# Performance work log

Hardware: AMD Instinct MI355X
Metric: run time of the kernel (lower is better)

The kernel has to match this reference:

```python
import jax, jax.numpy as jnp
import numpy as np

HEAD_SIZE = 64
EMBED_DIM = 1024
N_HEAD = EMBED_DIM // HEAD_SIZE
BATCH, SEQ = 8, 2048


def wkv6(r, k, v, w, u, s):
    # r,k,v,w: (B,T,H,D); u: (H,D); s: (B,H,D,D) indexed state[j,i] (j: key dim, i: value dim)
    decay = jnp.exp(-jnp.exp(w))  # RWKV-6 CUDA kernel computes exp(-exp(w)) per channel/step

    def step(state, inp):
        r_t, k_t, v_t, d_t = inp  # each (B,H,D)
        kv = k_t[..., :, None] * v_t[..., None, :]  # (B,H,D,D)
        y_t = jnp.einsum('bhj,bhji->bhi', r_t, state + u[..., :, None] * kv)
        state = d_t[..., :, None] * state + kv
        return state, y_t

    xs = tuple(jnp.moveaxis(t, 1, 0) for t in (r, k, v, decay))  # time-major (T,B,H,D)
    s_final, y = jax.lax.scan(step, s, xs)
    return jnp.moveaxis(y, 0, 1), s_final  # (B,T,H,D), (B,H,D,D)


def setup_inputs() -> dict:
    key = jax.random.key(0)
    ks = jax.random.split(key, 20)
    C, H, D = EMBED_DIM, N_HEAD, HEAD_SIZE
    f = jnp.float32
    inp = {
        'x': jax.random.normal(ks[0], (BATCH, SEQ, C), f),
        'x_last': jax.random.normal(ks[1], (BATCH, SEQ, C), f),
        's': jnp.zeros((BATCH, H, D, D), f),
        'miu_x': jax.random.uniform(ks[2], (1, 1, C), f),
        'lambda_': jax.random.uniform(ks[3], (5, 1, 1, C), f),
        'A': jax.random.normal(ks[4], (C, 160), f) * 0.01,
        'B_lora': jax.random.normal(ks[5], (5, 32, C), f) * 0.01,
        'time_decay_miu': jax.random.uniform(ks[6], (1, 1, C), f, minval=-6.0, maxval=-0.5),
        'td_A': jax.random.normal(ks[7], (C, 64), f) * 0.01,
        'td_B': jax.random.normal(ks[8], (64, C), f) * 0.01,
        'u': jax.random.normal(ks[9], (H, D), f) * 0.5,
        'W_k': jax.random.normal(ks[10], (C, C), f) * (0.05 / C ** 0.5),
        'W_v': jax.random.normal(ks[11], (C, C), f) * (0.5 / C ** 0.5),
        'W_r': jax.random.normal(ks[12], (C, C), f) * (0.5 / C ** 0.5),
        'W_o': jax.random.normal(ks[13], (C, C), f) * (0.5 / C ** 0.5),
        'W_g1': jax.random.normal(ks[14], (C, 160), f) * 0.01,
        'W_g2': jax.random.normal(ks[15], (160, C), f) * 0.01,
        'gn_gamma': jnp.ones((C,), f),
        'gn_beta': jnp.zeros((C,), f),
    }
    return inp


def reference(x, x_last, s, miu_x, lambda_, A, B_lora, time_decay_miu, td_A, td_B, u,
              W_k, W_v, W_r, W_o, W_g1, W_g2, gn_gamma, gn_beta):
    Bsz, T, C = x.shape
    H, D = C // HEAD_SIZE, HEAD_SIZE
    x_raw = x
    # ddlerp: token-shift mix with data-dependent mus from batched LoRA
    b_a = x_last - x
    xl = x + b_a * miu_x
    # NB: source uses a raw .view(5, B*T, 32) (no transpose) -- replicate exactly with reshape
    t1 = jnp.tanh(xl @ A).reshape(5, Bsz * T, 32)
    miu = lambda_ + jnp.einsum('fmk,fkc->fmc', t1, B_lora).reshape(5, Bsz, T, C)
    xdd = x[None] + b_a[None] * miu  # (5,B,T,C)
    w0, k0, v0, r0, g0 = xdd[0], xdd[1], xdd[2], xdd[3], xdd[4]
    # decay LoRA
    w = time_decay_miu + jnp.tanh(w0 @ td_A) @ td_B  # (B,T,C)
    k = (k0 @ W_k.T) * jnp.exp(jnp.minimum(w, 0.0))
    v = v0 @ W_v.T
    r = r0 @ W_r.T
    g = jnp.tanh(g0 @ W_g1) @ W_g2
    rh, kh, vh, wh = (t.reshape(Bsz, T, H, D) for t in (r, k, v, w))
    y, s_new = wkv6(rh, kh, vh, wh, u, s)
    # GroupNorm over (B*T, n_head groups of head_size), eps = 1e-5 * n_head
    y = y.reshape(Bsz * T, H, D)
    eps = 1e-5 * H
    mu = y.mean(axis=-1, keepdims=True)
    var = y.var(axis=-1, keepdims=True)
    yn = (y - mu) / jnp.sqrt(var + eps)
    yn = yn * gn_gamma.reshape(H, D) + gn_beta.reshape(H, D)
    yn = yn.reshape(Bsz, T, C)
    out = (yn * g) @ W_o.T
    return out, x_raw, s_new
```

## Files before the change

kernel.cpp:

```cpp
#include <hip/hip_runtime.h>
#include <hip/hip_bf16.h>

namespace {

typedef __attribute__((ext_vector_type(8))) short short8x;
typedef __attribute__((ext_vector_type(4))) float f32x4;

__device__ __forceinline__ float bf2f(unsigned short h) {
    return __uint_as_float(((unsigned int)h) << 16);
}
__device__ __forceinline__ unsigned short f2bf(float f) {
    __hip_bfloat16 h = __float2bfloat16(f);
    return *reinterpret_cast<unsigned short*>(&h);
}

enum { ACT_NONE = 0, ACT_TANH = 1 };
enum { EPI_NONE = 0, EPI_KSCALE = 1, EPI_ADDVEC = 2 };

template <int ACT, int EPI, int SBF>
__launch_bounds__(256) __global__
void gemm_mfma(int Npad, int K, int Nreal, int Cstride,
               const unsigned short* __restrict__ A,
               const unsigned short* __restrict__ B,
               float* __restrict__ Cf, unsigned short* __restrict__ Cb,
               const float* __restrict__ epi)
{
    __shared__ unsigned short as_[128 * 32];
    __shared__ unsigned short bs_[128 * 32];
    const int tid = threadIdx.x;
    const int lane = tid & 63;
    const int wave = tid >> 6;
    const int m0 = blockIdx.y << 7;
    const int n0 = blockIdx.x << 7;
    const int wm = (wave >> 1) << 6;
    const int wn = (wave & 1) << 6;

    f32x4 acc[4][4];
    const f32x4 zero = {0.f, 0.f, 0.f, 0.f};
#pragma unroll
    for (int i = 0; i < 4; ++i)
#pragma unroll
        for (int j = 0; j < 4; ++j) acc[i][j] = zero;

    const int sr = tid >> 2;
    const int sc4 = tid & 3;

    for (int k0 = 0; k0 < K; k0 += 32) {
        const uint4 a0 = *(const uint4*)(A + (size_t)(m0 + sr) * K + k0 + sc4 * 8);
        const uint4 a1 = *(const uint4*)(A + (size_t)(m0 + 64 + sr) * K + k0 + sc4 * 8);
        const uint4 b0 = *(const uint4*)(B + (size_t)(n0 + sr) * K + k0 + sc4 * 8);
        const uint4 b1 = *(const uint4*)(B + (size_t)(n0 + 64 + sr) * K + k0 + sc4 * 8);
        __syncthreads();
        {
            int r = sr, p = sc4 ^ ((r >> 1) & 3);
            *(uint4*)&as_[r * 32 + p * 8] = a0;
            *(uint4*)&bs_[r * 32 + p * 8] = b0;
            r = 64 + sr; p = sc4 ^ ((r >> 1) & 3);
            *(uint4*)&as_[r * 32 + p * 8] = a1;
            *(uint4*)&bs_[r * 32 + p * 8] = b1;
        }
        __syncthreads();
        const int q = lane >> 4;
        const int l15 = lane & 15;
        short8x af[4], bfr[4];
#pragma unroll
        for (int i = 0; i < 4; ++i) {
            const int m = wm + (i << 4) + l15;
            const int pa = q ^ ((m >> 1) & 3);
            af[i] = *(const short8x*)&as_[m * 32 + pa * 8];
            const int n = wn + (i << 4) + l15;
            const int pb = q ^ ((n >> 1) & 3);
            bfr[i] = *(const short8x*)&bs_[n * 32 + pb * 8];
        }
#pragma unroll
        for (int i = 0; i < 4; ++i)
#pragma unroll
            for (int j = 0; j < 4; ++j)
                acc[i][j] = __builtin_amdgcn_mfma_f32_16x16x32_bf16(af[i], bfr[j], acc[i][j], 0, 0, 0);
    }

    const int q = lane >> 4;
    const int cn = lane & 15;
#pragma unroll
    for (int i = 0; i < 4; ++i) {
#pragma unroll
        for (int j = 0; j < 4; ++j) {
#pragma unroll
            for (int rr = 0; rr < 4; ++rr) {
                const int row = m0 + wm + (i << 4) + (q << 2) + rr;
                const int col = n0 + wn + (j << 4) + cn;
                if (col >= Nreal) continue;
                float v = acc[i][j][rr];
                if constexpr (ACT == ACT_TANH) v = tanhf(v);
                if constexpr (EPI == EPI_KSCALE)
                    v *= __expf(fminf(epi[(size_t)row * 1024 + col], 0.f));
                if constexpr (EPI == EPI_ADDVEC) v += epi[col];
                if constexpr (SBF) Cb[(size_t)row * Cstride + col] = f2bf(v);
                else               Cf[(size_t)row * Cstride + col] = v;
            }
        }
    }
}

__launch_bounds__(256) __global__
void mix_k(const float* __restrict__ x, const float* __restrict__ xla,
           const float* __restrict__ mux, unsigned short* __restrict__ out)
{
    const size_t idx = ((size_t)blockIdx.x * 256 + threadIdx.x) * 4;
    const int c = (int)(idx & 1023);
    const float4 xv = *(const float4*)(x + idx);
    const float4 xl = *(const float4*)(xla + idx);
    const float4 mu = *(const float4*)(mux + c);
    ushort4 o;
    o.x = f2bf(xv.x + (xl.x - xv.x) * mu.x);
    o.y = f2bf(xv.y + (xl.y - xv.y) * mu.y);
    o.z = f2bf(xv.z + (xl.z - xv.z) * mu.z);
    o.w = f2bf(xv.w + (xl.w - xv.w) * mu.w);
    *(ushort4*)(out + idx) = o;
}

__launch_bounds__(256) __global__
void convert_k(const float* __restrict__ src, unsigned short* __restrict__ dst)
{
    const size_t idx = ((size_t)blockIdx.x * 256 + threadIdx.x) * 4;
    const float4 v = *(const float4*)(src + idx);
    ushort4 o;
    o.x = f2bf(v.x); o.y = f2bf(v.y); o.z = f2bf(v.z); o.w = f2bf(v.w);
    *(ushort4*)(dst + idx) = o;
}

__launch_bounds__(256) __global__
void transpose_k(const float* __restrict__ src, unsigned short* __restrict__ dst,
                 int K, int Nsrc)
{
    const int k = blockIdx.x * 256 + threadIdx.x;
    const int n = blockIdx.y;
    if (k < K)
        dst[(size_t)n * K + k] = (n < Nsrc) ? f2bf(src[(size_t)k * Nsrc + n]) : (unsigned short)0;
}

__launch_bounds__(256) __global__
void xdd_k(const float* __restrict__ x, const float* __restrict__ xla,
           const unsigned short* __restrict__ t1, const float* __restrict__ blora,
           const float* __restrict__ lam, unsigned short* __restrict__ out, int f)
{
    __shared__ float sh[4][32];
    const int tid = threadIdx.x;
    const int m0 = blockIdx.x << 2;
    if (tid < 128) {
        const int r = tid >> 5, kk = tid & 31;
        sh[r][kk] = bf2f(t1[(size_t)f * 524288 + (size_t)(m0 + r) * 32 + kk]);
    }
    __syncthreads();
    const int c0 = tid << 2;
    const float* bl = blora + f * 32768 + c0;
    float dot[4][4];
#pragma unroll
    for (int r = 0; r < 4; ++r)
#pragma unroll
        for (int j = 0; j < 4; ++j) dot[r][j] = 0.f;
    for (int kk = 0; kk < 32; ++kk) {
        const float4 b4 = *(const float4*)(bl + (size_t)kk * 1024);
#pragma unroll
        for (int r = 0; r < 4; ++r) {
            const float tv = sh[r][kk];
            dot[r][0] = fmaf(tv, b4.x, dot[r][0]);
            dot[r][1] = fmaf(tv, b4.y, dot[r][1]);
            dot[r][2] = fmaf(tv, b4.z, dot[r][2]);
            dot[r][3] = fmaf(tv, b4.w, dot[r][3]);
        }
    }
    const float4 l4 = *(const float4*)(lam + f * 1024 + c0);
#pragma unroll
    for (int r = 0; r < 4; ++r) {
        const size_t idx = (size_t)(m0 + r) * 1024 + c0;
        const float4 xv = *(const float4*)(x + idx);
        const float4 xl = *(const float4*)(xla + idx);
        ushort4 o;
        o.x = f2bf(xv.x + (xl.x - xv.x) * (l4.x + dot[r][0]));
        o.y = f2bf(xv.y + (xl.y - xv.y) * (l4.y + dot[r][1]));
        o.z = f2bf(xv.z + (xl.z - xv.z) * (l4.z + dot[r][2]));
        o.w = f2bf(xv.w + (xl.w - xv.w) * (l4.w + dot[r][3]));
        *(ushort4*)(out + idx) = o;
    }
}

__launch_bounds__(256) __global__
void zero_k(float4* __restrict__ p)
{
    const float4 z = {0.f, 0.f, 0.f, 0.f};
    p[(size_t)blockIdx.x * 256 + threadIdx.x] = z;
}

#define WKV_LOAD(RX, KX, WX, VV, T0)                                          \
    do {                                                                      \
        const size_t ti_ = tbase + (size_t)((T0) + ttl) * 1024;               \
        RX = r[ti_]; KX = k[ti_]; WX = w[ti_];                                \
        _Pragma("unroll")                                                     \
        for (int tt = 0; tt < 8; ++tt)                                        \
            VV[tt] = v[cbase + (size_t)((T0) + tt) * 1024];                   \
    } while (0)

#define WKV_CHUNK(RX, KX, WX, VV, T0)                                         \
    do {                                                                      \
        const float rr_ = bf2f(RX);                                           \
        const float kk_ = bf2f(KX);                                           \
        const float dd_ = __expf(-__expf(WX));                                \
        float4 tup_;                                                          \
        tup_.x = rr_; tup_.y = kk_; tup_.z = dd_; tup_.w = rr_ * kk_ * uj;    \
        __builtin_amdgcn_wave_barrier();    \
        sh[l] = tup_;                                                         \
        __builtin_amdgcn_wave_barrier();        \
        _Pragma("unroll")                                                     \
        for (int tt = 0; tt < 8; ++tt) {                                      \
            const float vi_ = bf2f(VV[tt]);                                   \
            float ya0_ = 0.f, ya1_ = 0.f, yb_ = 0.f;                          \
            _Pragma("unroll")                                                 \
            for (int jj = 0; jj < 8; ++jj) {                                  \
                const float4 t4_ = sh[(tt << 3) + jj];                        \
                const float sj_ = s[jj];                                      \
                if (jj & 1) ya1_ = fmaf(t4_.x, sj_, ya1_);                    \
                else        ya0_ = fmaf(t4_.x, sj_, ya0_);                    \
                yb_ += t4_.w;                                                 \
                s[jj] = fmaf(t4_.z, sj_, t4_.y * vi_);                        \
            }                                                                 \
            unsafeAtomicAdd(&y[cbase + (size_t)((T0) + tt) * 1024],           \
                            ya0_ + ya1_ + yb_ * vi_);                         \
        }                                                                     \
    } while (0)

__launch_bounds__(64) __global__
void wkv_k(const unsigned short* __restrict__ r, const unsigned short* __restrict__ k,
           const unsigned short* __restrict__ v, const float* __restrict__ w,
           const float* __restrict__ u, const float* __restrict__ s_in,
           float* __restrict__ y, float* __restrict__ s_out)
{
    const int blk = blockIdx.x;
    const int bh = blk >> 3;
    const int jc = blk & 7;
    const int h = bh & 15;
    const int l = threadIdx.x;
    const int jbase = jc << 3;

    float s[8];
    const size_t sb = (size_t)bh * 4096;
#pragma unroll
    for (int jj = 0; jj < 8; ++jj) s[jj] = s_in[sb + (size_t)(jbase + jj) * 64 + l];

    const int ttl = l >> 3;
    const int jl = l & 7;
    const float uj = u[(h << 6) + jbase + jl];

    __shared__ float4 sh[64];

    const size_t cbase = (size_t)(bh >> 4) * (2048 * 1024) + (h << 6) + l;
    const size_t tbase = (size_t)(bh >> 4) * (2048 * 1024) + (h << 6) + jbase + jl;

    unsigned short rA, kA; float wA; unsigned short vA[8];
    unsigned short rB, kB; float wB; unsigned short vB[8];

    WKV_LOAD(rA, kA, wA, vA, 0);
    for (int c = 0; c < 256; c += 2) {
        WKV_LOAD(rB, kB, wB, vB, (c + 1) * 8);
        WKV_CHUNK(rA, kA, wA, vA, c * 8);
        if (c + 2 < 256) WKV_LOAD(rA, kA, wA, vA, (c + 2) * 8);
        WKV_CHUNK(rB, kB, wB, vB, (c + 1) * 8);
    }
#pragma unroll
    for (int jj = 0; jj < 8; ++jj) s_out[sb + (size_t)(jbase + jj) * 64 + l] = s[jj];
}

__launch_bounds__(256) __global__
void gn_k(const float* __restrict__ y0,
          const unsigned short* __restrict__ g, const float* __restrict__ gam,
          const float* __restrict__ bet, unsigned short* __restrict__ z)
{
    const int tid = threadIdx.x;
    const size_t row = blockIdx.x;
    const int c0 = tid << 2;
    const size_t idx = row * 1024 + c0;
    const float4 a = *(const float4*)(y0 + idx);
    const float yv0 = a.x, yv1 = a.y, yv2 = a.z, yv3 = a.w;
    float sm = yv0 + yv1 + yv2 + yv3;
    float q = yv0 * yv0 + yv1 * yv1 + yv2 * yv2 + yv3 * yv3;
#pragma unroll
    for (int off = 1; off < 16; off <<= 1) {
        sm += __shfl_xor(sm, off, 64);
        q += __shfl_xor(q, off, 64);
    }
    const float mean = sm * (1.f / 64.f);
    const float var = q * (1.f / 64.f) - mean * mean;
    const float rstd = rsqrtf(var + 1.6e-4f);
    const float4 gm = *(const float4*)(gam + c0);
    const float4 bt = *(const float4*)(bet + c0);
    const ushort4 gg = *(const ushort4*)(g + idx);
    ushort4 o;
    o.x = f2bf(((yv0 - mean) * rstd * gm.x + bt.x) * bf2f(gg.x));
    o.y = f2bf(((yv1 - mean) * rstd * gm.y + bt.y) * bf2f(gg.y));
    o.z = f2bf(((yv2 - mean) * rstd * gm.z + bt.z) * bf2f(gg.z));
    o.w = f2bf(((yv3 - mean) * rstd * gm.w + bt.w) * bf2f(gg.w));
    *(ushort4*)(z + idx) = o;
}

__launch_bounds__(256) __global__
void copy_k(const float4* __restrict__ src, float4* __restrict__ dst)
{
    const size_t i = (size_t)blockIdx.x * 256 + threadIdx.x;
    dst[i] = src[i];
}

}

extern "C" void kernel_launch(void* const* d_in, const int* in_sizes, int n_in,
                              void* d_out, int out_size, void* d_ws, size_t ws_size,
                              hipStream_t stream)
{
    (void)in_sizes; (void)n_in; (void)out_size; (void)ws_size;
    const float* x     = (const float*)d_in[0];
    const float* xla   = (const float*)d_in[1];
    const float* s_in  = (const float*)d_in[2];
    const float* mux   = (const float*)d_in[3];
    const float* lam   = (const float*)d_in[4];
    const float* Amat  = (const float*)d_in[5];
    const float* blora = (const float*)d_in[6];
    const float* tdmu  = (const float*)d_in[7];
    const float* tdA   = (const float*)d_in[8];
    const float* tdB   = (const float*)d_in[9];
    const float* u     = (const float*)d_in[10];
    const float* Wk    = (const float*)d_in[11];
    const float* Wv    = (const float*)d_in[12];
    const float* Wr    = (const float*)d_in[13];
    const float* Wo    = (const float*)d_in[14];
    const float* Wg1   = (const float*)d_in[15];
    const float* Wg2   = (const float*)d_in[16];
    const float* gam   = (const float*)d_in[17];
    const float* bet   = (const float*)d_in[18];

    float* out  = (float*)d_out;
    float* xraw = out + 16777216;
    float* snew = out + 2 * 16777216;

    char* ws = (char*)d_ws;
    unsigned short* mixb   = (unsigned short*)(ws);
    unsigned short* xddb   = (unsigned short*)(ws + 33554432);
    unsigned short* t1     = (unsigned short*)(ws + 67108864);
    unsigned short* tanh64 = (unsigned short*)(ws + 72351744);
    unsigned short* tanhg  = (unsigned short*)(ws + 74448896);
    unsigned short* kbuf   = (unsigned short*)(ws + 79691776);
    unsigned short* vbuf   = (unsigned short*)(ws + 113246208);
    unsigned short* rbuf   = (unsigned short*)(ws + 146800640);
    unsigned short* gbuf   = (unsigned short*)(ws + 180355072);
    unsigned short* wkt    = (unsigned short*)(ws + 213909504);
    unsigned short* wvt    = (unsigned short*)(ws + 216006656);
    unsigned short* wrt    = (unsigned short*)(ws + 218103808);
    unsigned short* wot    = (unsigned short*)(ws + 220200960);
    unsigned short* at_    = (unsigned short*)(ws + 222298112);
    unsigned short* tdat   = (unsigned short*)(ws + 222822400);
    unsigned short* tdbt   = (unsigned short*)(ws + 223084544);
    unsigned short* wg1t   = (unsigned short*)(ws + 223215616);
    unsigned short* wg2t   = (unsigned short*)(ws + 223739904);

    float* w  = out;
    float* y0 = xraw;

    convert_k<<<1024, 256, 0, stream>>>(Wk, wkt);
    convert_k<<<1024, 256, 0, stream>>>(Wv, wvt);
    convert_k<<<1024, 256, 0, stream>>>(Wr, wrt);
    convert_k<<<1024, 256, 0, stream>>>(Wo, wot);
    transpose_k<<<dim3(4, 256), 256, 0, stream>>>(Amat, at_, 1024, 160);
    transpose_k<<<dim3(4, 128), 256, 0, stream>>>(tdA, tdat, 1024, 64);
    transpose_k<<<dim3(1, 1024), 256, 0, stream>>>(tdB, tdbt, 64, 1024);
    transpose_k<<<dim3(4, 256), 256, 0, stream>>>(Wg1, wg1t, 1024, 160);
    transpose_k<<<dim3(1, 1024), 256, 0, stream>>>(Wg2, wg2t, 160, 1024);

    mix_k<<<16384, 256, 0, stream>>>(x, xla, mux, mixb);
    gemm_mfma<ACT_TANH, EPI_NONE, 1><<<dim3(2, 128), 256, 0, stream>>>(
        256, 1024, 160, 160, mixb, at_, nullptr, t1, nullptr);

    xdd_k<<<4096, 256, 0, stream>>>(x, xla, t1, blora, lam, xddb, 0);
    gemm_mfma<ACT_TANH, EPI_NONE, 1><<<dim3(1, 128), 256, 0, stream>>>(
        128, 1024, 64, 64, xddb, tdat, nullptr, tanh64, nullptr);
    gemm_mfma<ACT_NONE, EPI_ADDVEC, 0><<<dim3(8, 128), 256, 0, stream>>>(
        1024, 64, 1024, 1024, tanh64, tdbt, w, nullptr, tdmu);

    xdd_k<<<4096, 256, 0, stream>>>(x, xla, t1, blora, lam, xddb, 1);
    gemm_mfma<ACT_NONE, EPI_KSCALE, 1><<<dim3(8, 128), 256, 0, stream>>>(
        1024, 1024, 1024, 1024, xddb, wkt, nullptr, kbuf, w);

    xdd_k<<<4096, 256, 0, stream>>>(x, xla, t1, blora, lam, xddb, 2);
    gemm_mfma<ACT_NONE, EPI_NONE, 1><<<dim3(8, 128), 256, 0, stream>>>(
        1024, 1024, 1024, 1024, xddb, wvt, nullptr, vbuf, nullptr);

    xdd_k<<<4096, 256, 0, stream>>>(x, xla, t1, blora, lam, xddb, 3);
    gemm_mfma<ACT_NONE, EPI_NONE, 1><<<dim3(8, 128), 256, 0, stream>>>(
        1024, 1024, 1024, 1024, xddb, wrt, nullptr, rbuf, nullptr);

    xdd_k<<<4096, 256, 0, stream>>>(x, xla, t1, blora, lam, xddb, 4);
    gemm_mfma<ACT_TANH, EPI_NONE, 1><<<dim3(2, 128), 256, 0, stream>>>(
        256, 1024, 160, 160, xddb, wg1t, nullptr, tanhg, nullptr);
    gemm_mfma<ACT_NONE, EPI_NONE, 1><<<dim3(8, 128), 256, 0, stream>>>(
        1024, 160, 1024, 1024, tanhg, wg2t, nullptr, gbuf, nullptr);

    zero_k<<<16384, 256, 0, stream>>>((float4*)y0);
    wkv_k<<<1024, 64, 0, stream>>>(rbuf, kbuf, vbuf, w, u, s_in, y0, snew);

    gn_k<<<16384, 256, 0, stream>>>(y0, gbuf, gam, bet, kbuf);

    gemm_mfma<ACT_NONE, EPI_NONE, 0><<<dim3(8, 128), 256, 0, stream>>>(
        1024, 1024, 1024, 1024, kbuf, wot, out, nullptr, nullptr);

    copy_k<<<16384, 256, 0, stream>>>((const float4*)x, (float4*)xraw);
}
```

Measured before the change: 1.389 ms.

## Precompute decay in separate kernel and drop LDS broadcast in WKV recurrence

A new elementwise kernel turns w into exp(-exp(w)) in place after the k GEMM has used w, so the recurrence no longer computes exponentials. The WKV kernel now has each lane load the 8 r/k/decay values for its j-slice as wide vector loads, replacing the per-wave LDS broadcast and its wave barriers. The u-bonus term is folded directly into the y accumulation. Block indexing is also remapped so the blocks sharing the same head are spread apart. This trades redundant broadcast global loads and more registers for fewer LDS round trips and barriers on the serial critical path, at the cost of one extra elementwise pass over w.

```diff
diff --git a/kernel.cpp b/kernel.cpp
--- a/kernel.cpp
+++ b/kernel.cpp
@@ -192,52 +192,75 @@
     p[(size_t)blockIdx.x * 256 + threadIdx.x] = z;
 }
 
-#define WKV_LOAD(RX, KX, WX, VV, T0)                                          \
+__launch_bounds__(256) __global__
+void decay_k(float* __restrict__ p)
+{
+    const size_t idx = ((size_t)blockIdx.x * 256 + threadIdx.x) * 4;
+    const float4 v = *(const float4*)(p + idx);
+    float4 o;
+    o.x = __expf(-__expf(v.x));
+    o.y = __expf(-__expf(v.y));
+    o.z = __expf(-__expf(v.z));
+    o.w = __expf(-__expf(v.w));
+    *(float4*)(p + idx) = o;
+}
+
+#define BF_LO(x) __uint_as_float((x) << 16)
+#define BF_HI(x) __uint_as_float((x) & 0xFFFF0000u)
+
+#define WKV_LOAD(RV, KV, DV, VVv, T0)                                         \
     do {                                                                      \
-        const size_t ti_ = tbase + (size_t)((T0) + ttl) * 1024;               \
-        RX = r[ti_]; KX = k[ti_]; WX = w[ti_];                                \
         _Pragma("unroll")                                                     \
-        for (int tt = 0; tt < 8; ++tt)                                        \
-            VV[tt] = v[cbase + (size_t)((T0) + tt) * 1024];                   \
+        for (int tt = 0; tt < 4; ++tt) {                                      \
+            const size_t o_ = (size_t)((T0) + tt) * 1024;                     \
+            RV[tt] = *(const uint4*)(rp + o_);                                \
+            KV[tt] = *(const uint4*)(kp + o_);                                \
+            DV[tt][0] = *(const float4*)(dp + o_);                            \
+            DV[tt][1] = *(const float4*)(dp + o_ + 4);                        \
+            VVv[tt] = vp[o_];                                                 \
+        }                                                                     \
     } while (0)
 
-#define WKV_CHUNK(RX, KX, WX, VV, T0)                                         \
+#define WKV_PROC(RV, KV, DV, VVv, T0)                                         \
     do {                                                                      \
-        const float rr_ = bf2f(RX);                                           \
-        const float kk_ = bf2f(KX);                                           \
-        const float dd_ = __expf(-__expf(WX));                                \
-        float4 tup_;                                                          \
-        tup_.x = rr_; tup_.y = kk_; tup_.z = dd_; tup_.w = rr_ * kk_ * uj;    \
-        __builtin_amdgcn_wave_barrier();    \
-        sh[l] = tup_;                                                         \
-        __builtin_amdgcn_wave_barrier();        \
         _Pragma("unroll")                                                     \
-        for (int tt = 0; tt < 8; ++tt) {                                      \
-            const float vi_ = bf2f(VV[tt]);                                   \
-            float ya0_ = 0.f, ya1_ = 0.f, yb_ = 0.f;                          \
+        for (int tt = 0; tt < 4; ++tt) {                                      \
+            const float vi_ = bf2f(VVv[tt]);                                  \
+            float rj[8], kj[8], dj[8];                                        \
+            rj[0] = BF_LO(RV[tt].x); rj[1] = BF_HI(RV[tt].x);                 \
+            rj[2] = BF_LO(RV[tt].y); rj[3] = BF_HI(RV[tt].y);                 \
+            rj[4] = BF_LO(RV[tt].z); rj[5] = BF_HI(RV[tt].z);                 \
+            rj[6] = BF_LO(RV[tt].w); rj[7] = BF_HI(RV[tt].w);                 \
+            kj[0] = BF_LO(KV[tt].x); kj[1] = BF_HI(KV[tt].x);                 \
+            kj[2] = BF_LO(KV[tt].y); kj[3] = BF_HI(KV[tt].y);                 \
+            kj[4] = BF_LO(KV[tt].z); kj[5] = BF_HI(KV[tt].z);                 \
+            kj[6] = BF_LO(KV[tt].w); kj[7] = BF_HI(KV[tt].w);                 \
+            dj[0] = DV[tt][0].x; dj[1] = DV[tt][0].y;                         \
+            dj[2] = DV[tt][0].z; dj[3] = DV[tt][0].w;                         \
+            dj[4] = DV[tt][1].x; dj[5] = DV[tt][1].y;                         \
+            dj[6] = DV[tt][1].z; dj[7] = DV[tt][1].w;                         \
+            float ya0_ = 0.f, ya1_ = 0.f;                                     \
             _Pragma("unroll")                                                 \
             for (int jj = 0; jj < 8; ++jj) {                                  \
-                const float4 t4_ = sh[(tt << 3) + jj];                        \
-                const float sj_ = s[jj];                                      \
-                if (jj & 1) ya1_ = fmaf(t4_.x, sj_, ya1_);                    \
-                else        ya0_ = fmaf(t4_.x, sj_, ya0_);                    \
-                yb_ += t4_.w;                                                 \
-                s[jj] = fmaf(t4_.z, sj_, t4_.y * vi_);                        \
+                const float t_ = kj[jj] * vi_;                                \
+                const float a_ = fmaf(u8[jj], t_, s[jj]);                     \
+                if (jj & 1) ya1_ = fmaf(rj[jj], a_, ya1_);                    \
+                else        ya0_ = fmaf(rj[jj], a_, ya0_);                    \
+                s[jj] = fmaf(dj[jj], s[jj], t_);                              \
             }                                                                 \
-            unsafeAtomicAdd(&y[cbase + (size_t)((T0) + tt) * 1024],           \
-                            ya0_ + ya1_ + yb_ * vi_);                         \
+            unsafeAtomicAdd(yp + (size_t)((T0) + tt) * 1024, ya0_ + ya1_);    \
         }                                                                     \
     } while (0)
 
 __launch_bounds__(64) __global__
 void wkv_k(const unsigned short* __restrict__ r, const unsigned short* __restrict__ k,
-           const unsigned short* __restrict__ v, const float* __restrict__ w,
+           const unsigned short* __restrict__ v, const float* __restrict__ d,
            const float* __restrict__ u, const float* __restrict__ s_in,
            float* __restrict__ y, float* __restrict__ s_out)
 {
     const int blk = blockIdx.x;
-    const int bh = blk >> 3;
-    const int jc = blk & 7;
+    const int bh = blk & 127;
+    const int jc = blk >> 7;
     const int h = bh & 15;
     const int l = threadIdx.x;
     const int jbase = jc << 3;
@@ -247,24 +270,26 @@
 #pragma unroll
     for (int jj = 0; jj < 8; ++jj) s[jj] = s_in[sb + (size_t)(jbase + jj) * 64 + l];
 
-    const int ttl = l >> 3;
-    const int jl = l & 7;
-    const float uj = u[(h << 6) + jbase + jl];
-
-    __shared__ float4 sh[64];
-
-    const size_t cbase = (size_t)(bh >> 4) * (2048 * 1024) + (h << 6) + l;
-    const size_t tbase = (size_t)(bh >> 4) * (2048 * 1024) + (h << 6) + jbase + jl;
-
-    unsigned short rA, kA; float wA; unsigned short vA[8];
-    unsigned short rB, kB; float wB; unsigned short vB[8];
-
-    WKV_LOAD(rA, kA, wA, vA, 0);
-    for (int c = 0; c < 256; c += 2) {
-        WKV_LOAD(rB, kB, wB, vB, (c + 1) * 8);
-        WKV_CHUNK(rA, kA, wA, vA, c * 8);
-        if (c + 2 < 256) WKV_LOAD(rA, kA, wA, vA, (c + 2) * 8);
-        WKV_CHUNK(rB, kB, wB, vB, (c + 1) * 8);
+    float u8[8];
+#pragma unroll
+    for (int jj = 0; jj < 8; ++jj) u8[jj] = u[(h << 6) + jbase + jj];
+
+    const size_t base = (size_t)(bh >> 4) * (2048 * 1024) + (h << 6);
+    const unsigned short* rp = r + base + jbase;
+    const unsigned short* kp = k + base + jbase;
+    const float*          dp = d + base + jbase;
+    const unsigned short* vp = v + base + l;
+    float*                yp = y + base + l;
+
+    uint4 rA[4], kA[4]; float4 dA[4][2]; unsigned short vA[4];
+    uint4 rB[4], kB[4]; float4 dB[4][2]; unsigned short vB[4];
+
+    WKV_LOAD(rA, kA, dA, vA, 0);
+    for (int c = 0; c < 512; c += 2) {
+        WKV_LOAD(rB, kB, dB, vB, (c + 1) * 4);
+        WKV_PROC(rA, kA, dA, vA, c * 4);
+        if (c + 2 < 512) WKV_LOAD(rA, kA, dA, vA, (c + 2) * 4);
+        WKV_PROC(rB, kB, dB, vB, (c + 1) * 4);
     }
 #pragma unroll
     for (int jj = 0; jj < 8; ++jj) s_out[sb + (size_t)(jbase + jj) * 64 + l] = s[jj];
@@ -387,6 +412,8 @@
     gemm_mfma<ACT_NONE, EPI_KSCALE, 1><<<dim3(8, 128), 256, 0, stream>>>(
         1024, 1024, 1024, 1024, xddb, wkt, nullptr, kbuf, w);
 
+    decay_k<<<16384, 256, 0, stream>>>(w);
+
     xdd_k<<<4096, 256, 0, stream>>>(x, xla, t1, blora, lam, xddb, 2);
     gemm_mfma<ACT_NONE, EPI_NONE, 1><<<dim3(8, 128), 256, 0, stream>>>(
         1024, 1024, 1024, 1024, xddb, wvt, nullptr, vbuf, nullptr);
```

After: 2.299 ms. +65.5%, slower.
